# Performance work log

Hardware: AMD Instinct MI355X
Metric: run time of the kernel (lower is better)

The kernel has to match this reference:

```python
import jax, jax.numpy as jnp
import numpy as np

N_NODES = 100000
N_EDGES = 1600000
D_FEAT = 512
HEADS = 8
UNITS1 = 8          # layer1: 8 heads x 8 units, concat -> 64
HIDDEN = HEADS * UNITS1
OUT_DIM = 16        # layer2: 8 heads x 16 units, avg -> 16
N_IDX = 10000
NEG_SLOPE = 0.2     # LeakyReLU slope used by GAT attention


def _gat_layer(x, edges, W, a_src, a_dst, merge):
    """One multi-head GAT layer.
    x: [N, F], edges: [E, 2] with (dst, src) columns,
    W: [F, H, U], a_src/a_dst: [H, U].
    """
    n = x.shape[0]
    dst = edges[:, 0]
    src = edges[:, 1]
    h = jnp.einsum('nf,fhu->nhu', x, W)                      # [N, H, U]
    # per-node attention score halves, then gather per edge (cheaper than
    # gathering full features first)
    s_src = jnp.einsum('nhu,hu->nh', h, a_src)               # [N, H]
    s_dst = jnp.einsum('nhu,hu->nh', h, a_dst)               # [N, H]
    e = s_dst[dst] + s_src[src]                              # [E, H]
    e = jnp.where(e > 0, e, NEG_SLOPE * e)                   # LeakyReLU
    # segment softmax over incoming edges of each dst node (stable)
    m = jax.ops.segment_max(e, dst, num_segments=n)          # [N, H]
    m = jnp.where(jnp.isfinite(m), m, 0.0)                   # empty segments
    ex = jnp.exp(e - m[dst])                                 # [E, H]
    denom = jax.ops.segment_sum(ex, dst, num_segments=n)     # [N, H]
    alpha = ex / jnp.maximum(denom[dst], 1e-9)               # [E, H]
    msg = h[src] * alpha[:, :, None]                         # [E, H, U]
    out = jax.ops.segment_sum(msg, dst, num_segments=n)      # [N, H, U]
    if merge == 'concat':
        return out.reshape(n, -1)                            # [N, H*U]
    return out.mean(axis=1)                                  # [N, U]


def setup_inputs() -> dict:
    key = jax.random.key(0)
    ks = jax.random.split(key, 9)
    node_states = jax.random.normal(ks[0], (N_NODES, D_FEAT), dtype=jnp.float32)
    edges = jax.random.randint(ks[1], (N_EDGES, 2), 0, N_NODES, dtype=jnp.int32).astype(jnp.int64)
    indices = jax.random.randint(ks[2], (N_IDX,), 0, N_NODES, dtype=jnp.int32).astype(jnp.int64)
    W1 = jax.random.normal(ks[3], (D_FEAT, HEADS, UNITS1), dtype=jnp.float32) / np.sqrt(D_FEAT)
    a1_src = jax.random.normal(ks[4], (HEADS, UNITS1), dtype=jnp.float32) / np.sqrt(UNITS1)
    a1_dst = jax.random.normal(ks[5], (HEADS, UNITS1), dtype=jnp.float32) / np.sqrt(UNITS1)
    W2 = jax.random.normal(ks[6], (HIDDEN, HEADS, OUT_DIM), dtype=jnp.float32) / np.sqrt(HIDDEN)
    a2_src = jax.random.normal(ks[7], (HEADS, OUT_DIM), dtype=jnp.float32) / np.sqrt(OUT_DIM)
    a2_dst = jax.random.normal(ks[8], (HEADS, OUT_DIM), dtype=jnp.float32) / np.sqrt(OUT_DIM)
    return {
        'node_states': node_states, 'edges': edges, 'indices': indices,
        'W1': W1, 'a1_src': a1_src, 'a1_dst': a1_dst,
        'W2': W2, 'a2_src': a2_src, 'a2_dst': a2_dst,
    }


def reference(node_states, edges, indices, W1, a1_src, a1_dst, W2, a2_src, a2_dst):
    # layer 1: concat merge + ELU nonlinearity (standard GAT hidden layer)
    x = _gat_layer(node_states, edges, W1, a1_src, a1_dst, merge='concat')
    x = jax.nn.elu(x)                                        # [N, 64]
    # layer 2: average merge, linear output logits
    out = _gat_layer(x, edges, W2, a2_src, a2_dst, merge='avg')  # [N, OUT_DIM]
    return jnp.take(out, indices, axis=0)                    # [N_IDX, OUT_DIM]
```

## Files before the change

### kernel.cpp

```cpp
#include <hip/hip_runtime.h>
#include <hip/hip_bf16.h>

#define NN 100000
#define NE 1600000
#define DF 512
#define NIDX 10000

#define NBKT 512
#define BKT_W 196
#define EDGES_PER_BKT_BLK 3125

typedef __attribute__((ext_vector_type(8))) short short8v;
typedef __attribute__((ext_vector_type(4))) float float4v;

__device__ __forceinline__ float eluf(float x) { return x > 0.f ? x : expm1f(x); }
__device__ __forceinline__ float lrelu(float x) { return x > 0.f ? x : 0.2f * x; }
__device__ __forceinline__ ushort f2bf(float f) {
  __hip_bfloat16 b = __float2bfloat16(f);
  return *(ushort*)&b;
}

__global__ __launch_bounds__(256) void prep_w_kernel(const float* __restrict__ W1,
                                                     ushort* __restrict__ Wt_hi, ushort* __restrict__ Wt_lo,
                                                     int* __restrict__ bkt_cnt) {
  if (blockIdx.x == 0) {
    bkt_cnt[threadIdx.x] = 0;
    bkt_cnt[threadIdx.x + 256] = 0;
  }
  int t = blockIdx.x * 256 + threadIdx.x;
  if (t >= DF * 64) return;
  int k = t >> 6, n = t & 63;
  float w = W1[t];
  ushort hi = f2bf(w);
  __hip_bfloat16 hb = *(__hip_bfloat16*)&hi;
  ushort lo = f2bf(w - __bfloat162float(hb));
  Wt_hi[(size_t)n * DF + k] = hi;
  Wt_lo[(size_t)n * DF + k] = lo;
}

#define AST 40
#define BST 40
__global__ __launch_bounds__(256) void gemm1_mfma(const float* __restrict__ x,
                                                  const ushort* __restrict__ Wt_hi, const ushort* __restrict__ Wt_lo,
                                                  const float* __restrict__ a1s, const float* __restrict__ a1d,
                                                  ushort* __restrict__ h1b, float* __restrict__ s_src,
                                                  float* __restrict__ s_dst) {
  __shared__ __align__(16) char smem[33280];
  ushort* As_hi = (ushort*)smem;
  ushort* As_lo = As_hi + 128 * AST;
  ushort* Bs_hi = As_lo + 128 * AST;
  ushort* Bs_lo = Bs_hi + 64 * BST;
  float* Cs = (float*)smem;

  const int tid = threadIdx.x;
  const int m0 = blockIdx.x * 128;
  const int wave = tid >> 6, l = tid & 63;
  const int wm = wave * 32;
  const int lm = l & 15, kg = (l >> 4) * 8;

  float4v acc[2][4];
#pragma unroll
  for (int i = 0; i < 2; ++i)
#pragma unroll
    for (int j = 0; j < 4; ++j) acc[i][j] = (float4v){0.f, 0.f, 0.f, 0.f};

  const int arow = tid >> 1;
  const int ac0 = (tid & 1) * 16;
  const int grow = m0 + arow;
  const int bn = tid & 63, bk = (tid >> 6) * 8;

  for (int k0 = 0; k0 < DF; k0 += 32) {
#pragma unroll
    for (int i = 0; i < 4; ++i) {
      float4 v = make_float4(0.f, 0.f, 0.f, 0.f);
      if (grow < NN) v = *(const float4*)&x[(size_t)grow * DF + k0 + ac0 + 4 * i];
      ushort4 h, lo;
      h.x = f2bf(v.x); h.y = f2bf(v.y); h.z = f2bf(v.z); h.w = f2bf(v.w);
      lo.x = f2bf(v.x - __bfloat162float(*(__hip_bfloat16*)&h.x));
      lo.y = f2bf(v.y - __bfloat162float(*(__hip_bfloat16*)&h.y));
      lo.z = f2bf(v.z - __bfloat162float(*(__hip_bfloat16*)&h.z));
      lo.w = f2bf(v.w - __bfloat162float(*(__hip_bfloat16*)&h.w));
      *(ushort4*)&As_hi[arow * AST + ac0 + 4 * i] = h;
      *(ushort4*)&As_lo[arow * AST + ac0 + 4 * i] = lo;
    }
    *(uint4*)&Bs_hi[bn * BST + bk] = *(const uint4*)&Wt_hi[(size_t)bn * DF + k0 + bk];
    *(uint4*)&Bs_lo[bn * BST + bk] = *(const uint4*)&Wt_lo[(size_t)bn * DF + k0 + bk];
    __syncthreads();

    short8v ah[2], al[2], bh[4], bl[4];
#pragma unroll
    for (int mt = 0; mt < 2; ++mt) {
      ah[mt] = *(const short8v*)&As_hi[(wm + mt * 16 + lm) * AST + kg];
      al[mt] = *(const short8v*)&As_lo[(wm + mt * 16 + lm) * AST + kg];
    }
#pragma unroll
    for (int nt = 0; nt < 4; ++nt) {
      bh[nt] = *(const short8v*)&Bs_hi[(nt * 16 + lm) * BST + kg];
      bl[nt] = *(const short8v*)&Bs_lo[(nt * 16 + lm) * BST + kg];
    }
#pragma unroll
    for (int mt = 0; mt < 2; ++mt)
#pragma unroll
      for (int nt = 0; nt < 4; ++nt) {
        acc[mt][nt] = __builtin_amdgcn_mfma_f32_16x16x32_bf16(ah[mt], bh[nt], acc[mt][nt], 0, 0, 0);
        acc[mt][nt] = __builtin_amdgcn_mfma_f32_16x16x32_bf16(ah[mt], bl[nt], acc[mt][nt], 0, 0, 0);
        acc[mt][nt] = __builtin_amdgcn_mfma_f32_16x16x32_bf16(al[mt], bh[nt], acc[mt][nt], 0, 0, 0);
      }
    __syncthreads();
  }

#pragma unroll
  for (int mt = 0; mt < 2; ++mt)
#pragma unroll
    for (int nt = 0; nt < 4; ++nt)
#pragma unroll
      for (int r = 0; r < 4; ++r)
        Cs[(wm + mt * 16 + (l >> 4) * 4 + r) * 65 + nt * 16 + lm] = acc[mt][nt][r];
  __syncthreads();

  {
    int row = tid >> 1, c0 = (tid & 1) * 32;
    int g = m0 + row;
    if (g < NN) {
      uint u[16];
#pragma unroll
      for (int j = 0; j < 16; ++j) {
        uint p0 = f2bf(Cs[row * 65 + c0 + 2 * j]);
        uint p1 = f2bf(Cs[row * 65 + c0 + 2 * j + 1]);
        u[j] = p0 | (p1 << 16);
      }
#pragma unroll
      for (int q = 0; q < 4; ++q)
        *(uint4*)&h1b[(size_t)g * 64 + c0 + 8 * q] = *(uint4*)&u[4 * q];
      int half = tid & 1;
      float4 ssv, ddv;
      float* ssp = &ssv.x;
      float* ddp = &ddv.x;
#pragma unroll
      for (int hq = 0; hq < 4; ++hq) {
        int hh = half * 4 + hq;
        float ss = 0.f, dd = 0.f;
#pragma unroll
        for (int u8 = 0; u8 < 8; ++u8) {
          float hv = Cs[row * 65 + hh * 8 + u8];
          ss = fmaf(hv, a1s[hh * 8 + u8], ss);
          dd = fmaf(hv, a1d[hh * 8 + u8], dd);
        }
        ssp[hq] = ss; ddp[hq] = dd;
      }
      *(float4*)&s_src[(size_t)g * 8 + half * 4] = ssv;
      *(float4*)&s_dst[(size_t)g * 8 + half * 4] = ddv;
    }
  }
}

__global__ __launch_bounds__(256) void gemm2_fused(const float* __restrict__ A, const float* __restrict__ B,
                                                   __hip_bfloat162* __restrict__ Cb,
                                                   const float* __restrict__ a2s, const float* __restrict__ a2d,
                                                   float* __restrict__ s_src, float* __restrict__ s_dst,
                                                   int M, int N, int K) {
  __shared__ float sm[2 * 32 * 68];
  float* As = sm;
  float* Bs = sm + 32 * 68;
  float* Cs = sm;
  const int tid = threadIdx.x;
  const int m0 = blockIdx.x * 64;
  const int n0 = blockIdx.y * 64;
  const int tx = tid & 15, ty = tid >> 4;
  float acc[4][4] = {};
  for (int k0 = 0; k0 < K; k0 += 32) {
    for (int j = tid; j < 512; j += 256) {
      int r = j >> 3, kq = j & 7;
      int row = m0 + r;
      float4 v = make_float4(0.f, 0.f, 0.f, 0.f);
      if (row < M) v = *(const float4*)&A[(size_t)row * K + k0 + kq * 4];
      v.x = eluf(v.x); v.y = eluf(v.y); v.z = eluf(v.z); v.w = eluf(v.w);
      As[(kq * 4 + 0) * 68 + r] = v.x; As[(kq * 4 + 1) * 68 + r] = v.y;
      As[(kq * 4 + 2) * 68 + r] = v.z; As[(kq * 4 + 3) * 68 + r] = v.w;
    }
    for (int j = tid; j < 512; j += 256) {
      int kr = j >> 4, nq = j & 15;
      *(float4*)&Bs[kr * 68 + nq * 4] = *(const float4*)&B[(size_t)(k0 + kr) * N + n0 + nq * 4];
    }
    __syncthreads();
#pragma unroll
    for (int kk = 0; kk < 32; ++kk) {
      float4 a4 = *(const float4*)&As[kk * 68 + ty * 4];
      float4 b4 = *(const float4*)&Bs[kk * 68 + tx * 4];
      float av[4] = {a4.x, a4.y, a4.z, a4.w};
      float bv[4] = {b4.x, b4.y, b4.z, b4.w};
#pragma unroll
      for (int i = 0; i < 4; ++i)
#pragma unroll
        for (int jj = 0; jj < 4; ++jj)
          acc[i][jj] = fmaf(av[i], bv[jj], acc[i][jj]);
    }
    __syncthreads();
  }
#pragma unroll
  for (int i = 0; i < 4; ++i) {
    int row = m0 + ty * 4 + i;
    if (row < M) {
      __hip_bfloat162 p0, p1;
      p0.x = __float2bfloat16(acc[i][0]); p0.y = __float2bfloat16(acc[i][1]);
      p1.x = __float2bfloat16(acc[i][2]); p1.y = __float2bfloat16(acc[i][3]);
      size_t base = ((size_t)row * N + n0 + tx * 4) >> 1;
      Cb[base] = p0; Cb[base + 1] = p1;
    }
#pragma unroll
    for (int jj = 0; jj < 4; ++jj)
      Cs[(ty * 4 + i) * 65 + tx * 4 + jj] = acc[i][jj];
  }
  __syncthreads();
  {
    int row = tid >> 2, q = tid & 3;
    int g = m0 + row;
    if (g < M) {
      int hh = (n0 >> 4) + q;
      float ss = 0.f, dd = 0.f;
#pragma unroll
      for (int u = 0; u < 16; ++u) {
        float v = Cs[row * 65 + q * 16 + u];
        ss = fmaf(v, a2s[hh * 16 + u], ss);
        dd = fmaf(v, a2d[hh * 16 + u], dd);
      }
      s_src[(size_t)g * 8 + hh] = ss;
      s_dst[(size_t)g * 8 + hh] = dd;
    }
  }
}

__global__ __launch_bounds__(256) void bkt_hist_kernel(const int2* __restrict__ edges, int* __restrict__ bkt_cnt) {
  __shared__ int h[NBKT];
  const int tid = threadIdx.x;
  h[tid] = 0; h[tid + 256] = 0;
  __syncthreads();
  const int i0 = blockIdx.x * EDGES_PER_BKT_BLK;
  const int i1 = min(i0 + EDGES_PER_BKT_BLK, NE);
  for (int i = i0 + tid; i < i1; i += 256) atomicAdd(&h[edges[i].x / BKT_W], 1);
  __syncthreads();
  if (h[tid]) atomicAdd(&bkt_cnt[tid], h[tid]);
  if (h[tid + 256]) atomicAdd(&bkt_cnt[tid + 256], h[tid + 256]);
}

__global__ __launch_bounds__(NBKT) void bkt_scan_kernel(const int* __restrict__ bkt_cnt, int* __restrict__ bkt_base,
                                                        int* __restrict__ bkt_cursor, int* __restrict__ row_off) {
  __shared__ int s[NBKT];
  int tid = threadIdx.x;
  int v = bkt_cnt[tid];
  s[tid] = v;
  __syncthreads();
  for (int off = 1; off < NBKT; off <<= 1) {
    int t = (tid >= off) ? s[tid - off] : 0;
    __syncthreads();
    s[tid] += t;
    __syncthreads();
  }
  int excl = s[tid] - v;
  bkt_base[tid] = excl;
  bkt_cursor[tid] = excl;
  if (tid == NBKT - 1) bkt_base[NBKT] = s[tid];
  if (tid == 0) row_off[NN] = NE;
}

__global__ __launch_bounds__(256) void bkt_reorder_kernel(const int2* __restrict__ edges, int* __restrict__ bkt_cursor,
                                                          uint* __restrict__ pairs) {
  __shared__ int h[NBKT];
  __shared__ int lbase[NBKT];
  __shared__ int cur[NBKT];
  const int tid = threadIdx.x;
  h[tid] = 0; h[tid + 256] = 0;
  __syncthreads();
  const int i0 = blockIdx.x * EDGES_PER_BKT_BLK;
  const int i1 = min(i0 + EDGES_PER_BKT_BLK, NE);
  for (int i = i0 + tid; i < i1; i += 256) atomicAdd(&h[edges[i].x / BKT_W], 1);
  __syncthreads();
#pragma unroll
  for (int q = 0; q < 2; ++q) {
    int b = tid + q * 256;
    int c = h[b];
    lbase[b] = c ? atomicAdd(&bkt_cursor[b], c) : 0;
    cur[b] = 0;
  }
  __syncthreads();
  for (int i = i0 + tid; i < i1; i += 256) {
    int2 e = edges[i];
    int bk = e.x / BKT_W;
    int r = atomicAdd(&cur[bk], 1);
    pairs[lbase[bk] + r] = ((uint)(e.x - bk * BKT_W) << 24) | (uint)e.y;
  }
}

__global__ __launch_bounds__(256) void bkt_build_kernel(const uint* __restrict__ pairs, const int* __restrict__ bkt_base,
                                                        int* __restrict__ row_off, int* __restrict__ ssrc) {
  __shared__ int hist[256];
  __shared__ int ts[256];
  __shared__ int cur[256];
  const int b = blockIdx.x, tid = threadIdx.x;
  const int d0 = b * BKT_W;
  if (d0 >= NN) return;
  const int nd = min(BKT_W, NN - d0);
  const int beg = bkt_base[b], end = bkt_base[b + 1];
  hist[tid] = 0;
  __syncthreads();
  for (int i = beg + tid; i < end; i += 256) atomicAdd(&hist[pairs[i] >> 24], 1);
  __syncthreads();
  int v = hist[tid];
  ts[tid] = v;
  __syncthreads();
  for (int off = 1; off < 256; off <<= 1) {
    int t = (tid >= off) ? ts[tid - off] : 0;
    __syncthreads();
    ts[tid] += t;
    __syncthreads();
  }
  int excl = ts[tid] - v;
  if (tid < nd) row_off[d0 + tid] = beg + excl;
  cur[tid] = beg + excl;
  __syncthreads();
  for (int i = beg + tid; i < end; i += 256) {
    uint p = pairs[i];
    int pos = atomicAdd(&cur[p >> 24], 1);
    ssrc[pos] = (int)(p & 0xFFFFFFu);
  }
}

__global__ __launch_bounds__(256) void agg1_kernel(const int* __restrict__ row_off, const int* __restrict__ srcs,
                                                   const float* __restrict__ s_src, const float* __restrict__ s_dst,
                                                   const __hip_bfloat16* __restrict__ hb, float* __restrict__ out, int n) {
  int wave = (blockIdx.x * 256 + threadIdx.x) >> 6;
  int lane = threadIdx.x & 63;
  if (wave >= n) return;
  int hh = lane >> 3;
  float sd = s_dst[(size_t)wave * 8 + hh];
  int beg = row_off[wave], end = row_off[wave + 1];
  float acc = 0.f, den = 0.f;
  int i = beg;
  for (; i + 4 <= end; i += 4) {
    int s0 = srcs[i], s1 = srcs[i + 1], s2 = srcs[i + 2], s3 = srcs[i + 3];
    float e0 = s_src[(size_t)s0 * 8 + hh];
    float e1 = s_src[(size_t)s1 * 8 + hh];
    float e2 = s_src[(size_t)s2 * 8 + hh];
    float e3 = s_src[(size_t)s3 * 8 + hh];
    float h0 = __bfloat162float(hb[(size_t)s0 * 64 + lane]);
    float h1 = __bfloat162float(hb[(size_t)s1 * 64 + lane]);
    float h2 = __bfloat162float(hb[(size_t)s2 * 64 + lane]);
    float h3 = __bfloat162float(hb[(size_t)s3 * 64 + lane]);
    float x0 = __expf(lrelu(sd + e0));
    float x1 = __expf(lrelu(sd + e1));
    float x2 = __expf(lrelu(sd + e2));
    float x3 = __expf(lrelu(sd + e3));
    den += (x0 + x1) + (x2 + x3);
    acc = fmaf(x0, h0, fmaf(x1, h1, fmaf(x2, h2, fmaf(x3, h3, acc))));
  }
  for (; i < end; ++i) {
    int s0 = srcs[i];
    float x0 = __expf(lrelu(sd + s_src[(size_t)s0 * 8 + hh]));
    den += x0;
    acc = fmaf(x0, __bfloat162float(hb[(size_t)s0 * 64 + lane]), acc);
  }
  out[(size_t)wave * 64 + lane] = acc / fmaxf(den, 1e-9f);
}

__global__ __launch_bounds__(256) void agg2_idx_kernel(const int* __restrict__ row_off, const int* __restrict__ srcs,
                                                       const float* __restrict__ s_src, const float* __restrict__ s_dst,
                                                       const __hip_bfloat162* __restrict__ h2b, const int* __restrict__ idx,
                                                       float* __restrict__ out, int ni) {
  int w = (blockIdx.x * 256 + threadIdx.x) >> 6;
  int lane = threadIdx.x & 63;
  if (w >= ni) return;
  int node = idx[w];
  int hh = lane >> 3, o2 = lane & 7;
  float sd = s_dst[(size_t)node * 8 + hh];
  int beg = row_off[node], end = row_off[node + 1];
  float a0 = 0.f, a1 = 0.f, den = 0.f;
  int i = beg;
  for (; i + 4 <= end; i += 4) {
    int s0 = srcs[i], s1 = srcs[i + 1], s2 = srcs[i + 2], s3 = srcs[i + 3];
    float e0 = s_src[(size_t)s0 * 8 + hh];
    float e1 = s_src[(size_t)s1 * 8 + hh];
    float e2 = s_src[(size_t)s2 * 8 + hh];
    float e3 = s_src[(size_t)s3 * 8 + hh];
    float2 v0 = __bfloat1622float2(h2b[(size_t)s0 * 64 + hh * 8 + o2]);
    float2 v1 = __bfloat1622float2(h2b[(size_t)s1 * 64 + hh * 8 + o2]);
    float2 v2 = __bfloat1622float2(h2b[(size_t)s2 * 64 + hh * 8 + o2]);
    float2 v3 = __bfloat1622float2(h2b[(size_t)s3 * 64 + hh * 8 + o2]);
    float x0 = __expf(lrelu(sd + e0));
    float x1 = __expf(lrelu(sd + e1));
    float x2 = __expf(lrelu(sd + e2));
    float x3 = __expf(lrelu(sd + e3));
    den += (x0 + x1) + (x2 + x3);
    a0 = fmaf(x0, v0.x, fmaf(x1, v1.x, fmaf(x2, v2.x, fmaf(x3, v3.x, a0))));
    a1 = fmaf(x0, v0.y, fmaf(x1, v1.y, fmaf(x2, v2.y, fmaf(x3, v3.y, a1))));
  }
  for (; i < end; ++i) {
    int s0 = srcs[i];
    float x0 = __expf(lrelu(sd + s_src[(size_t)s0 * 8 + hh]));
    float2 v0 = __bfloat1622float2(h2b[(size_t)s0 * 64 + hh * 8 + o2]);
    den += x0;
    a0 = fmaf(x0, v0.x, a0);
    a1 = fmaf(x0, v0.y, a1);
  }
  float r0 = a0 / fmaxf(den, 1e-9f);
  float r1 = a1 / fmaxf(den, 1e-9f);
  for (int m = 8; m < 64; m <<= 1) {
    r0 += __shfl_xor(r0, m, 64);
    r1 += __shfl_xor(r1, m, 64);
  }
  if (lane < 8) {
    float2 wv = make_float2(r0 * 0.125f, r1 * 0.125f);
    *(float2*)&out[(size_t)w * 16 + lane * 2] = wv;
  }
}

extern "C" void kernel_launch(void* const* d_in, const int* in_sizes, int n_in,
                              void* d_out, int out_size, void* d_ws, size_t ws_size,
                              hipStream_t stream) {
  const float* x   = (const float*)d_in[0];
  const int2* edges = (const int2*)d_in[1];
  const int* indices = (const int*)d_in[2];
  const float* W1  = (const float*)d_in[3];
  const float* a1s = (const float*)d_in[4];
  const float* a1d = (const float*)d_in[5];
  const float* W2  = (const float*)d_in[6];
  const float* a2s = (const float*)d_in[7];
  const float* a2d = (const float*)d_in[8];
  float* out = (float*)d_out;

  char* ws = (char*)d_ws;
  size_t off = 0;
  auto alloc = [&](size_t bytes) {
    void* p = ws + off;
    off = (off + bytes + 255) & ~(size_t)255;
    return p;
  };
  float* s1src = (float*)alloc((size_t)NN * 8 * 4);
  float* s1dst = (float*)alloc((size_t)NN * 8 * 4);
  float* out1  = (float*)alloc((size_t)NN * 64 * 4);
  ushort* h1b  = (ushort*)alloc((size_t)NN * 64 * 2);
  __hip_bfloat162* h2b = (__hip_bfloat162*)alloc((size_t)NN * 128 * 2);
  int* row_off = (int*)alloc(((size_t)NN + 1) * 4);
  int* ssrc    = (int*)alloc((size_t)NE * 4);
  uint* pairs  = (uint*)alloc((size_t)NE * 4);
  ushort* Wt_hi = (ushort*)alloc((size_t)DF * 64 * 2);
  ushort* Wt_lo = (ushort*)alloc((size_t)DF * 64 * 2);
  int* bkt_cnt    = (int*)alloc(NBKT * 4);
  int* bkt_base   = (int*)alloc((NBKT + 1) * 4);
  int* bkt_cursor = (int*)alloc(NBKT * 4);

  dim3 b256(256);
  prep_w_kernel<<<dim3((DF * 64 + 255) / 256), b256, 0, stream>>>(W1, Wt_hi, Wt_lo, bkt_cnt);
  gemm1_mfma<<<dim3((NN + 127) / 128), b256, 0, stream>>>(x, Wt_hi, Wt_lo, a1s, a1d, h1b, s1src, s1dst);
  bkt_hist_kernel<<<dim3(NBKT), b256, 0, stream>>>(edges, bkt_cnt);
  bkt_scan_kernel<<<dim3(1), dim3(NBKT), 0, stream>>>(bkt_cnt, bkt_base, bkt_cursor, row_off);
  bkt_reorder_kernel<<<dim3(NBKT), b256, 0, stream>>>(edges, bkt_cursor, pairs);
  bkt_build_kernel<<<dim3(NBKT), b256, 0, stream>>>(pairs, bkt_base, row_off, ssrc);
  agg1_kernel<<<dim3(NN / 4), b256, 0, stream>>>(row_off, ssrc, s1src, s1dst, (const __hip_bfloat16*)h1b, out1, NN);
  gemm2_fused<<<dim3((NN + 63) / 64, 2), b256, 0, stream>>>(out1, W2, h2b, a2s, a2d, s1src, s1dst, NN, 128, 64);
  agg2_idx_kernel<<<dim3((NIDX * 64 + 255) / 256), b256, 0, stream>>>(row_off, ssrc, s1src, s1dst, h2b, indices, out, NIDX);
}
```

Measured before the change: 263.7 us.

## Load GEMM1 operands straight into MFMA registers with register prefetch, dropping LDS staging

The first-layer GEMM no longer stages A and B tiles through shared memory with two barriers per k-step. Each lane now loads its fp32 x fragment directly from global memory, splitting it into bf16 hi/lo in registers by bit truncation, and reads W hi/lo fragments directly from global (L2-resident). The next k-slice of x is prefetched into registers so loads overlap the MFMAs. This removes LDS traffic and syncs, but the hi/lo split now truncates instead of rounding to nearest, which slightly changes numerics, and global access patterns are less coalesced.

Result: slower. 365.5 us (+38.6%).

```diff
diff --git a/kernel.cpp b/kernel.cpp
--- a/kernel.cpp
+++ b/kernel.cpp
@@ -38,25 +38,17 @@
   Wt_lo[(size_t)n * DF + k] = lo;
 }
 
-#define AST 40
-#define BST 40
 __global__ __launch_bounds__(256) void gemm1_mfma(const float* __restrict__ x,
                                                   const ushort* __restrict__ Wt_hi, const ushort* __restrict__ Wt_lo,
                                                   const float* __restrict__ a1s, const float* __restrict__ a1d,
                                                   ushort* __restrict__ h1b, float* __restrict__ s_src,
                                                   float* __restrict__ s_dst) {
-  __shared__ __align__(16) char smem[33280];
-  ushort* As_hi = (ushort*)smem;
-  ushort* As_lo = As_hi + 128 * AST;
-  ushort* Bs_hi = As_lo + 128 * AST;
-  ushort* Bs_lo = Bs_hi + 64 * BST;
-  float* Cs = (float*)smem;
-
+  __shared__ float Cs[128 * 65];
   const int tid = threadIdx.x;
-  const int m0 = blockIdx.x * 128;
+  const int mb = blockIdx.x * 128;
   const int wave = tid >> 6, l = tid & 63;
-  const int wm = wave * 32;
-  const int lm = l & 15, kg = (l >> 4) * 8;
+  const int m0 = mb + wave * 32;
+  const int lm = l & 15, kq = l >> 4, kg = kq * 8;
 
   float4v acc[2][4];
 #pragma unroll
@@ -64,40 +56,51 @@
 #pragma unroll
     for (int j = 0; j < 4; ++j) acc[i][j] = (float4v){0.f, 0.f, 0.f, 0.f};
 
-  const int arow = tid >> 1;
-  const int ac0 = (tid & 1) * 16;
-  const int grow = m0 + arow;
-  const int bn = tid & 63, bk = (tid >> 6) * 8;
-
+  const int r0 = m0 + lm;
+  const int r1 = m0 + 16 + lm;
+  const bool v0 = r0 < NN, v1 = r1 < NN;
+  const float* xp0 = x + (size_t)r0 * DF + kg;
+  const float* xp1 = x + (size_t)r1 * DF + kg;
+  const float4 z4 = make_float4(0.f, 0.f, 0.f, 0.f);
+
+  float4 a_cur[2][2];
+  a_cur[0][0] = v0 ? *(const float4*)(xp0) : z4;
+  a_cur[0][1] = v0 ? *(const float4*)(xp0 + 4) : z4;
+  a_cur[1][0] = v1 ? *(const float4*)(xp1) : z4;
+  a_cur[1][1] = v1 ? *(const float4*)(xp1 + 4) : z4;
+
+#pragma unroll 2
   for (int k0 = 0; k0 < DF; k0 += 32) {
-#pragma unroll
-    for (int i = 0; i < 4; ++i) {
-      float4 v = make_float4(0.f, 0.f, 0.f, 0.f);
-      if (grow < NN) v = *(const float4*)&x[(size_t)grow * DF + k0 + ac0 + 4 * i];
-      ushort4 h, lo;
-      h.x = f2bf(v.x); h.y = f2bf(v.y); h.z = f2bf(v.z); h.w = f2bf(v.w);
-      lo.x = f2bf(v.x - __bfloat162float(*(__hip_bfloat16*)&h.x));
-      lo.y = f2bf(v.y - __bfloat162float(*(__hip_bfloat16*)&h.y));
-      lo.z = f2bf(v.z - __bfloat162float(*(__hip_bfloat16*)&h.z));
-      lo.w = f2bf(v.w - __bfloat162float(*(__hip_bfloat16*)&h.w));
-      *(ushort4*)&As_hi[arow * AST + ac0 + 4 * i] = h;
-      *(ushort4*)&As_lo[arow * AST + ac0 + 4 * i] = lo;
-    }
-    *(uint4*)&Bs_hi[bn * BST + bk] = *(const uint4*)&Wt_hi[(size_t)bn * DF + k0 + bk];
-    *(uint4*)&Bs_lo[bn * BST + bk] = *(const uint4*)&Wt_lo[(size_t)bn * DF + k0 + bk];
-    __syncthreads();
-
-    short8v ah[2], al[2], bh[4], bl[4];
+    const int k1 = (k0 + 32 < DF) ? (k0 + 32) : k0;
+    float4 a_nxt[2][2];
+    a_nxt[0][0] = v0 ? *(const float4*)(xp0 + k1) : z4;
+    a_nxt[0][1] = v0 ? *(const float4*)(xp0 + k1 + 4) : z4;
+    a_nxt[1][0] = v1 ? *(const float4*)(xp1 + k1) : z4;
+    a_nxt[1][1] = v1 ? *(const float4*)(xp1 + k1 + 4) : z4;
+
+    short8v bh[4], bl[4];
+#pragma unroll
+    for (int nt = 0; nt < 4; ++nt) {
+      bh[nt] = *(const short8v*)&Wt_hi[(size_t)(nt * 16 + lm) * DF + k0 + kg];
+      bl[nt] = *(const short8v*)&Wt_lo[(size_t)(nt * 16 + lm) * DF + k0 + kg];
+    }
+
+    short8v ah[2], al[2];
 #pragma unroll
     for (int mt = 0; mt < 2; ++mt) {
-      ah[mt] = *(const short8v*)&As_hi[(wm + mt * 16 + lm) * AST + kg];
-      al[mt] = *(const short8v*)&As_lo[(wm + mt * 16 + lm) * AST + kg];
-    }
-#pragma unroll
-    for (int nt = 0; nt < 4; ++nt) {
-      bh[nt] = *(const short8v*)&Bs_hi[(nt * 16 + lm) * BST + kg];
-      bl[nt] = *(const short8v*)&Bs_lo[(nt * 16 + lm) * BST + kg];
-    }
+      const float* fp = (const float*)&a_cur[mt][0];
+#pragma unroll
+      for (int c = 0; c < 8; ++c) {
+        float f = fp[c];
+        uint u = __float_as_uint(f);
+        ushort hi = (ushort)(u >> 16);
+        float hf = __uint_as_float(u & 0xFFFF0000u);
+        ushort lo = (ushort)(__float_as_uint(f - hf) >> 16);
+        ah[mt][c] = (short)hi;
+        al[mt][c] = (short)lo;
+      }
+    }
+
 #pragma unroll
     for (int mt = 0; mt < 2; ++mt)
 #pragma unroll
@@ -106,7 +109,11 @@
         acc[mt][nt] = __builtin_amdgcn_mfma_f32_16x16x32_bf16(ah[mt], bl[nt], acc[mt][nt], 0, 0, 0);
         acc[mt][nt] = __builtin_amdgcn_mfma_f32_16x16x32_bf16(al[mt], bh[nt], acc[mt][nt], 0, 0, 0);
       }
-    __syncthreads();
+
+#pragma unroll
+    for (int mt = 0; mt < 2; ++mt)
+#pragma unroll
+      for (int j = 0; j < 2; ++j) a_cur[mt][j] = a_nxt[mt][j];
   }
 
 #pragma unroll
@@ -115,12 +122,12 @@
     for (int nt = 0; nt < 4; ++nt)
 #pragma unroll
       for (int r = 0; r < 4; ++r)
-        Cs[(wm + mt * 16 + (l >> 4) * 4 + r) * 65 + nt * 16 + lm] = acc[mt][nt][r];
+        Cs[(wave * 32 + mt * 16 + kq * 4 + r) * 65 + nt * 16 + lm] = acc[mt][nt][r];
   __syncthreads();
 
   {
     int row = tid >> 1, c0 = (tid & 1) * 32;
-    int g = m0 + row;
+    int g = mb + row;
     if (g < NN) {
       uint u[16];
 #pragma unroll
```
